# Performance work log

Hardware: AMD Instinct MI355X
Metric: run time of the kernel (lower is better)

The kernel has to match this reference:

```python
import jax, jax.numpy as jnp
import numpy as np

D_MODEL = 1024
OUTPUT_DIM = 1024
NUM_HEADS = 16
HEAD_DIM = D_MODEL // NUM_HEADS


def _xavier(key, shape):
    fan_in, fan_out = shape[1], shape[0]
    limit = float(np.sqrt(6.0 / (fan_in + fan_out)))
    return jax.random.uniform(key, shape, jnp.float32, -limit, limit)


def setup_inputs() -> dict:
    key = jax.random.key(0)
    k_h, k_q, k_k, k_o = jax.random.split(key, 4)
    H = jax.random.normal(k_h, (2, 2048, D_MODEL), dtype=jnp.float32)
    # nn.Linear weights are [out, in]; xavier_uniform on weights, default (uniform) biases left as zeros-equivalent
    Wq = _xavier(k_q, (D_MODEL, D_MODEL))
    bq = jnp.zeros((D_MODEL,), jnp.float32)
    Wk = _xavier(k_k, (D_MODEL, D_MODEL))
    bk = jnp.zeros((D_MODEL,), jnp.float32)
    Wo = _xavier(k_o, (OUTPUT_DIM, D_MODEL))
    bo = jnp.zeros((OUTPUT_DIM,), jnp.float32)
    return {"H": H, "Wq": Wq, "bq": bq, "Wk": Wk, "bk": bk, "Wo": Wo, "bo": bo}


def reference(H, Wq, bq, Wk, bk, Wo, bo):
    B, S, _ = H.shape
    Q = H @ Wq.T + bq  # [B,S,D]
    K = H @ Wk.T + bk
    # split heads -> [B,nh,S,hd]
    Qh = Q.reshape(B, S, NUM_HEADS, HEAD_DIM).transpose(0, 2, 1, 3)
    Kh = K.reshape(B, S, NUM_HEADS, HEAD_DIM).transpose(0, 2, 1, 3)
    Vh = H.reshape(B, S, NUM_HEADS, HEAD_DIM).transpose(0, 2, 1, 3)
    scale = 1.0 / jnp.sqrt(jnp.float32(HEAD_DIM))
    A = jnp.einsum('bhqd,bhkd->bhqk', Qh, Kh) * scale  # [B,nh,S,S]
    A = jax.nn.softmax(A, axis=-1)
    out = jnp.einsum('bhqk,bhkd->bhqd', A, Vh)  # [B,nh,S,hd]
    out = out.transpose(0, 2, 1, 3).reshape(B, S, D_MODEL)
    return out @ Wo.T + bo
```

## Files before the change

### kernel.cpp

```cpp
#include <hip/hip_runtime.h>
#include <stdint.h>

#define BB 2
#define SS 2048
#define DD 1024
#define NH 16
#define HD 64
#define MM 4096

typedef __bf16 bf16x8 __attribute__((ext_vector_type(8)));
typedef __bf16 bf16x4 __attribute__((ext_vector_type(4)));
typedef float  f32x4  __attribute__((ext_vector_type(4)));

__device__ __forceinline__ unsigned short f2bf(float f) {
    __bf16 h = (__bf16)f;
    return __builtin_bit_cast(unsigned short, h);
}

__device__ __forceinline__ void async_cp16(const void* g, const void* l) {
    __builtin_amdgcn_global_load_lds(
        (const __attribute__((address_space(1))) void*)(uintptr_t)g,
        (__attribute__((address_space(3))) void*)(uint32_t)(uintptr_t)l,
        16, 0, 0);
}

__device__ __forceinline__ f32x4 mfma16(bf16x8 a, bf16x8 b, f32x4 c) {
    return __builtin_amdgcn_mfma_f32_16x16x32_bf16(a, b, c, 0, 0, 0);
}

__global__ __launch_bounds__(256) void k_prep(const float* __restrict__ H,
                                              const float* __restrict__ Wq,
                                              const float* __restrict__ Wk,
                                              const float* __restrict__ Wo,
                                              unsigned short* __restrict__ Hb,
                                              unsigned short* __restrict__ Vt,
                                              unsigned short* __restrict__ Wqb,
                                              unsigned short* __restrict__ Wkb,
                                              unsigned short* __restrict__ Wob) {
    __shared__ float tile[128][68];
    const int bx = blockIdx.x;
    const int t = threadIdx.x;
    if (bx >= 512) {
        int g = bx - 512;
        const float* src; unsigned short* dst; int base;
        if (g < 512)       { src = Wq; dst = Wqb; base = g; }
        else if (g < 1024) { src = Wk; dst = Wkb; base = g - 512; }
        else               { src = Wo; dst = Wob; base = g - 1024; }
        int i = (base * 256 + t) * 8;
        float4 a = *(const float4*)(src + i);
        float4 b = *(const float4*)(src + i + 4);
        unsigned short o[8];
        o[0] = f2bf(a.x); o[1] = f2bf(a.y); o[2] = f2bf(a.z); o[3] = f2bf(a.w);
        o[4] = f2bf(b.x); o[5] = f2bf(b.y); o[6] = f2bf(b.z); o[7] = f2bf(b.w);
        *(ulonglong2*)(dst + i) = *(ulonglong2*)o;
        return;
    }
    const int sb = bx & 15, h = (bx >> 4) & 15, b = bx >> 8;
    const int col4 = t & 15;
    const int srow0 = t >> 4;
#pragma unroll
    for (int p = 0; p < 8; ++p) {
        int s = p * 16 + srow0;
        float4 v = *(const float4*)(H + (size_t)(b * SS + sb * 128 + s) * DD + h * HD + col4 * 4);
        *(float4*)&tile[s][col4 * 4] = v;
    }
    __syncthreads();
#pragma unroll
    for (int it = 0; it < 4; ++it) {
        int task = it * 256 + t;
        int s = task >> 3;
        int dg = task & 7;
        unsigned short pk[8];
#pragma unroll
        for (int j = 0; j < 8; ++j) pk[j] = f2bf(tile[s][dg * 8 + j]);
        *(ulonglong2*)(Hb + (size_t)(b * SS + sb * 128 + s) * DD + h * HD + dg * 8) = *(ulonglong2*)pk;
    }
#pragma unroll
    for (int it = 0; it < 4; ++it) {
        int task = it * 256 + t;
        int d = task >> 4;
        int sg = task & 15;
        unsigned short pk[8];
#pragma unroll
        for (int j = 0; j < 8; ++j) pk[j] = f2bf(tile[sg * 8 + j][d]);
        *(ulonglong2*)(Vt + (size_t)((b * NH + h) * HD + d) * SS + sb * 128 + sg * 8) = *(ulonglong2*)pk;
    }
}

template <int TM, bool BF16OUT>
__device__ __forceinline__ void gemm_body(const unsigned short* __restrict__ A,
                                          const unsigned short* __restrict__ Bt,
                                          const float* __restrict__ bias,
                                          void* __restrict__ Cp, float oscale) {
    constexpr int MT = TM / 32;
    constexpr int AR = (TM * 4) / 256;
    __shared__ unsigned short lsA[2][TM * 32];
    __shared__ unsigned short lsB[2][128 * 32];
    const int tid = threadIdx.x;
    const int lane = tid & 63;
    const int w = tid >> 6;
    const int wm = w & 1, wn = w >> 1;
    const int r = lane & 15, quad = lane >> 4;
    const int mBase = blockIdx.y * TM;
    const int nBase = blockIdx.x * 128;

    const unsigned short* gA[AR]; uint laOff[AR];
#pragma unroll
    for (int t = 0; t < AR; ++t) {
        int l = t * 256 + tid;
        int c = l ^ ((l >> 3) & 7);
        int row = c >> 2, kc = c & 3;
        gA[t] = A + (size_t)(mBase + row) * 1024 + kc * 8;
        laOff[t] = l * 8;
    }
    const unsigned short* gB[2]; uint lbOff[2];
#pragma unroll
    for (int t = 0; t < 2; ++t) {
        int l = t * 256 + tid;
        int c = l ^ ((l >> 3) & 7);
        int row = c >> 2, kc = c & 3;
        gB[t] = Bt + (size_t)(nBase + row) * 1024 + kc * 8;
        lbOff[t] = l * 8;
    }
    uint aOff[MT], bOff[4];
#pragma unroll
    for (int mt = 0; mt < MT; ++mt) {
        int rowA = wm * (TM / 2) + mt * 16 + r;
        int c = rowA * 4 + quad;
        aOff[mt] = (uint)((c ^ ((c >> 3) & 7)) * 8);
    }
#pragma unroll
    for (int nt = 0; nt < 4; ++nt) {
        int rowB = wn * 64 + nt * 16 + r;
        int c = rowB * 4 + quad;
        bOff[nt] = (uint)((c ^ ((c >> 3) & 7)) * 8);
    }

    f32x4 acc[MT][4];
#pragma unroll
    for (int i = 0; i < MT; ++i)
#pragma unroll
        for (int j = 0; j < 4; ++j) acc[i][j] = f32x4{0.f, 0.f, 0.f, 0.f};

    auto stage = [&](int buf) {
#pragma unroll
        for (int t = 0; t < AR; ++t) { async_cp16(gA[t], &lsA[buf][laOff[t]]); gA[t] += 32; }
#pragma unroll
        for (int t = 0; t < 2; ++t)  { async_cp16(gB[t], &lsB[buf][lbOff[t]]); gB[t] += 32; }
    };

    stage(0);
    for (int kb = 0; kb < 32; ++kb) {
        const int cur = kb & 1;
        __syncthreads();
        if (kb + 1 < 32) stage(cur ^ 1);

        bf16x8 af[MT], bf[4];
#pragma unroll
        for (int mt = 0; mt < MT; ++mt) af[mt] = *(const bf16x8*)&lsA[cur][aOff[mt]];
#pragma unroll
        for (int nt = 0; nt < 4; ++nt)  bf[nt] = *(const bf16x8*)&lsB[cur][bOff[nt]];
#pragma unroll
        for (int mt = 0; mt < MT; ++mt)
#pragma unroll
            for (int nt = 0; nt < 4; ++nt)
                acc[mt][nt] = mfma16(af[mt], bf[nt], acc[mt][nt]);
    }

    float bv[4];
#pragma unroll
    for (int nt = 0; nt < 4; ++nt) bv[nt] = bias[nBase + wn * 64 + nt * 16 + r];
#pragma unroll
    for (int mt = 0; mt < MT; ++mt)
#pragma unroll
        for (int nt = 0; nt < 4; ++nt) {
            int colg = nBase + wn * 64 + nt * 16 + r;
#pragma unroll
            for (int reg = 0; reg < 4; ++reg) {
                int rowg = mBase + wm * (TM / 2) + mt * 16 + quad * 4 + reg;
                float v = (acc[mt][nt][reg] + bv[nt]) * oscale;
                if (BF16OUT)
                    ((unsigned short*)Cp)[(size_t)rowg * 1024 + colg] = f2bf(v);
                else
                    ((float*)Cp)[(size_t)rowg * 1024 + colg] = v;
            }
        }
}

#define QSCALE 0.1803368801111137f

__global__ __launch_bounds__(256) void k_gemm_qk(const unsigned short* __restrict__ Hb,
                                                 const unsigned short* __restrict__ Wqb,
                                                 const unsigned short* __restrict__ Wkb,
                                                 const float* __restrict__ bq,
                                                 const float* __restrict__ bk,
                                                 unsigned short* __restrict__ Q,
                                                 unsigned short* __restrict__ K) {
    const unsigned short* Bt = blockIdx.z ? Wkb : Wqb;
    const float* bias = blockIdx.z ? bk : bq;
    unsigned short* C = blockIdx.z ? K : Q;
    float os = blockIdx.z ? 1.0f : QSCALE;
    gemm_body<128, true>(Hb, Bt, bias, C, os);
}

__global__ __launch_bounds__(256) void k_gemm_out(const unsigned short* __restrict__ Ctx,
                                                  const unsigned short* __restrict__ Wob,
                                                  const float* __restrict__ bo,
                                                  float* __restrict__ Out) {
    gemm_body<64, false>(Ctx, Wob, bo, Out, 1.0f);
}

__global__ __launch_bounds__(256) void k_attn(const unsigned short* __restrict__ Q,
                                              const unsigned short* __restrict__ K,
                                              const unsigned short* __restrict__ Vt,
                                              unsigned short* __restrict__ Ctx) {
    __shared__ unsigned short lsK[2][64 * 64];
    __shared__ unsigned short lsV[2][64 * 64];
    __shared__ unsigned short lsP[4 * 32 * 64];
    const int tid = threadIdx.x;
    const int lane = tid & 63;
    const int w = tid >> 6;
    const int r = lane & 15, quad = lane >> 4;
    const int qb = blockIdx.x, h = blockIdx.y, b = blockIdx.z;

    bf16x8 aq[2][2];
#pragma unroll
    for (int sub = 0; sub < 2; ++sub) {
        const int qrow = qb * 128 + w * 32 + sub * 16 + r;
        const size_t qoff = (size_t)(b * SS + qrow) * DD + h * HD;
        aq[sub][0] = *(const bf16x8*)(Q + qoff + quad * 8);
        aq[sub][1] = *(const bf16x8*)(Q + qoff + 32 + quad * 8);
    }

    f32x4 accO[2][4];
#pragma unroll
    for (int sub = 0; sub < 2; ++sub)
#pragma unroll
        for (int nt = 0; nt < 4; ++nt) accO[sub][nt] = f32x4{0.f, 0.f, 0.f, 0.f};
    float lsum[2][4] = {{0.f, 0.f, 0.f, 0.f}, {0.f, 0.f, 0.f, 0.f}};

    const unsigned short* gK[2]; const unsigned short* gV[2]; uint lO[2];
#pragma unroll
    for (int t = 0; t < 2; ++t) {
        int l = t * 256 + tid;
        int c = l ^ ((l >> 3) & 7);
        int row = c >> 3, kc = c & 7;
        int srow = 4 * (row & 15) + (row >> 4);
        gK[t] = K + (size_t)(b * SS + srow) * DD + h * HD + kc * 8;
        gV[t] = Vt + (size_t)((b * NH + h) * HD + row) * SS + kc * 8;
        lO[t] = l * 8;
    }
    uint off[2][4];
#pragma unroll
    for (int t = 0; t < 2; ++t)
#pragma unroll
        for (int nt = 0; nt < 4; ++nt) {
            int rowX = nt * 16 + r;
            int c = rowX * 8 + t * 4 + quad;
            off[t][nt] = (uint)((c ^ ((c >> 3) & 7)) * 8);
        }
    uint pw[4], pr[2];
#pragma unroll
    for (int reg = 0; reg < 4; ++reg) {
        int prow = quad * 4 + reg;
        pw[reg] = (uint)(prow * 64 + ((r >> 1) ^ (prow & 7)) * 8 + (r & 1) * 4);
    }
#pragma unroll
    for (int t = 0; t < 2; ++t)
        pr[t] = (uint)(r * 64 + ((4 * t + quad) ^ (r & 7)) * 8);
    unsigned short* Pw = lsP + w * 2048;

    auto stage = [&](int buf) {
#pragma unroll
        for (int t = 0; t < 2; ++t) {
            async_cp16(gK[t], &lsK[buf][lO[t]]); gK[t] += 64 * DD;
            async_cp16(gV[t], &lsV[buf][lO[t]]); gV[t] += 64;
        }
    };

    stage(0);
    for (int kt = 0; kt < 32; ++kt) {
        const int cur = kt & 1;
        __syncthreads();
        if (kt + 1 < 32) stage(cur ^ 1);

        f32x4 s[2][4];
#pragma unroll
        for (int sub = 0; sub < 2; ++sub)
#pragma unroll
            for (int nt = 0; nt < 4; ++nt) s[sub][nt] = f32x4{0.f, 0.f, 0.f, 0.f};
#pragma unroll
        for (int t = 0; t < 2; ++t)
#pragma unroll
            for (int nt = 0; nt < 4; ++nt) {
                bf16x8 bk = *(const bf16x8*)&lsK[cur][off[t][nt]];
                s[0][nt] = mfma16(aq[0][t], bk, s[0][nt]);
                s[1][nt] = mfma16(aq[1][t], bk, s[1][nt]);
            }

#pragma unroll
        for (int sub = 0; sub < 2; ++sub)
#pragma unroll
            for (int reg = 0; reg < 4; ++reg) {
                float p0 = __builtin_amdgcn_exp2f(s[sub][0][reg]);
                float p1 = __builtin_amdgcn_exp2f(s[sub][1][reg]);
                float p2 = __builtin_amdgcn_exp2f(s[sub][2][reg]);
                float p3 = __builtin_amdgcn_exp2f(s[sub][3][reg]);
                lsum[sub][reg] += (p0 + p1) + (p2 + p3);
                bf16x4 pk = {(__bf16)p0, (__bf16)p1, (__bf16)p2, (__bf16)p3};
                *(bf16x4*)&Pw[sub * 1024 + pw[reg]] = pk;
            }

#pragma unroll
        for (int t = 0; t < 2; ++t) {
            bf16x8 ap0 = *(const bf16x8*)&Pw[pr[t]];
            bf16x8 ap1 = *(const bf16x8*)&Pw[1024 + pr[t]];
#pragma unroll
            for (int nt = 0; nt < 4; ++nt) {
                bf16x8 bv = *(const bf16x8*)&lsV[cur][off[t][nt]];
                accO[0][nt] = mfma16(ap0, bv, accO[0][nt]);
                accO[1][nt] = mfma16(ap1, bv, accO[1][nt]);
            }
        }
    }

#pragma unroll
    for (int sub = 0; sub < 2; ++sub) {
        float linv[4];
#pragma unroll
        for (int reg = 0; reg < 4; ++reg) {
            float l = lsum[sub][reg];
            l += __shfl_xor(l, 1);
            l += __shfl_xor(l, 2);
            l += __shfl_xor(l, 4);
            l += __shfl_xor(l, 8);
            linv[reg] = 1.0f / l;
        }
#pragma unroll
        for (int nt = 0; nt < 4; ++nt) {
            int d = nt * 16 + r;
#pragma unroll
            for (int reg = 0; reg < 4; ++reg) {
                int qr = qb * 128 + w * 32 + sub * 16 + quad * 4 + reg;
                Ctx[(size_t)(b * SS + qr) * DD + h * HD + d] = f2bf(accO[sub][nt][reg] * linv[reg]);
            }
        }
    }
}

extern "C" void kernel_launch(void* const* d_in, const int* in_sizes, int n_in,
                              void* d_out, int out_size, void* d_ws, size_t ws_size,
                              hipStream_t stream) {
    (void)in_sizes; (void)n_in; (void)out_size; (void)ws_size;
    const float* H  = (const float*)d_in[0];
    const float* Wq = (const float*)d_in[1];
    const float* bq = (const float*)d_in[2];
    const float* Wk = (const float*)d_in[3];
    const float* bk = (const float*)d_in[4];
    const float* Wo = (const float*)d_in[5];
    const float* bo = (const float*)d_in[6];
    float* Out = (float*)d_out;

    char* ws = (char*)d_ws;
    unsigned short* Hb  = (unsigned short*)(ws);
    unsigned short* Qb  = (unsigned short*)(ws + 8388608);
    unsigned short* Kb  = (unsigned short*)(ws + 16777216);
    unsigned short* Ctx = (unsigned short*)(ws + 25165824);
    unsigned short* Vt  = (unsigned short*)(ws + 33554432);
    unsigned short* Wqb = (unsigned short*)(ws + 41943040);
    unsigned short* Wkb = (unsigned short*)(ws + 44040192);
    unsigned short* Wob = (unsigned short*)(ws + 46137344);

    k_prep<<<dim3(2048), dim3(256), 0, stream>>>(H, Wq, Wk, Wo, Hb, Vt, Wqb, Wkb, Wob);
    k_gemm_qk<<<dim3(8, 32, 2), dim3(256), 0, stream>>>(Hb, Wqb, Wkb, bq, bk, Qb, Kb);
    k_attn<<<dim3(16, NH, BB), dim3(256), 0, stream>>>(Qb, Kb, Vt, Ctx);
    k_gemm_out<<<dim3(8, 64, 1), dim3(256), 0, stream>>>(Ctx, Wob, bo, Out);
}
```

Before: 181.3 us.

## Double GEMM K-tile to 64 and load attention K/V directly to registers

The GEMM body now stages 64-wide K slices instead of 32, halving the number of barrier-separated iterations and doubling the MFMA work per sync. The attention kernel drops the shared-memory staging of K and V and has each wave load its K and V fragments straight from global memory into registers, prefetching the next K tile. This removes the per-tile __syncthreads and LDS traffic. In exchange, each of the four waves fetches the same K/V data separately, so global/L2 traffic rises, and both register pressure and GEMM LDS usage grow.

```diff
diff --git a/kernel.cpp b/kernel.cpp
--- a/kernel.cpp
+++ b/kernel.cpp
@@ -93,9 +93,9 @@
                                           const float* __restrict__ bias,
                                           void* __restrict__ Cp, float oscale) {
     constexpr int MT = TM / 32;
-    constexpr int AR = (TM * 4) / 256;
-    __shared__ unsigned short lsA[2][TM * 32];
-    __shared__ unsigned short lsB[2][128 * 32];
+    constexpr int AR = TM / 32;
+    __shared__ unsigned short lsA[2][TM * 64];
+    __shared__ unsigned short lsB[2][128 * 64];
     const int tid = threadIdx.x;
     const int lane = tid & 63;
     const int w = tid >> 6;
@@ -109,31 +109,34 @@
     for (int t = 0; t < AR; ++t) {
         int l = t * 256 + tid;
         int c = l ^ ((l >> 3) & 7);
-        int row = c >> 2, kc = c & 3;
+        int row = c >> 3, kc = c & 7;
         gA[t] = A + (size_t)(mBase + row) * 1024 + kc * 8;
         laOff[t] = l * 8;
     }
-    const unsigned short* gB[2]; uint lbOff[2];
-#pragma unroll
-    for (int t = 0; t < 2; ++t) {
+    const unsigned short* gB[4]; uint lbOff[4];
+#pragma unroll
+    for (int t = 0; t < 4; ++t) {
         int l = t * 256 + tid;
         int c = l ^ ((l >> 3) & 7);
-        int row = c >> 2, kc = c & 3;
+        int row = c >> 3, kc = c & 7;
         gB[t] = Bt + (size_t)(nBase + row) * 1024 + kc * 8;
         lbOff[t] = l * 8;
     }
-    uint aOff[MT], bOff[4];
-#pragma unroll
-    for (int mt = 0; mt < MT; ++mt) {
-        int rowA = wm * (TM / 2) + mt * 16 + r;
-        int c = rowA * 4 + quad;
-        aOff[mt] = (uint)((c ^ ((c >> 3) & 7)) * 8);
-    }
-#pragma unroll
-    for (int nt = 0; nt < 4; ++nt) {
-        int rowB = wn * 64 + nt * 16 + r;
-        int c = rowB * 4 + quad;
-        bOff[nt] = (uint)((c ^ ((c >> 3) & 7)) * 8);
+    uint aOff[2][MT], bOff[2][4];
+#pragma unroll
+    for (int hh = 0; hh < 2; ++hh) {
+#pragma unroll
+        for (int mt = 0; mt < MT; ++mt) {
+            int rowA = wm * (TM / 2) + mt * 16 + r;
+            int c = rowA * 8 + hh * 4 + quad;
+            aOff[hh][mt] = (uint)((c ^ ((c >> 3) & 7)) * 8);
+        }
+#pragma unroll
+        for (int nt = 0; nt < 4; ++nt) {
+            int rowB = wn * 64 + nt * 16 + r;
+            int c = rowB * 8 + hh * 4 + quad;
+            bOff[hh][nt] = (uint)((c ^ ((c >> 3) & 7)) * 8);
+        }
     }
 
     f32x4 acc[MT][4];
@@ -144,27 +147,30 @@
 
     auto stage = [&](int buf) {
 #pragma unroll
-        for (int t = 0; t < AR; ++t) { async_cp16(gA[t], &lsA[buf][laOff[t]]); gA[t] += 32; }
-#pragma unroll
-        for (int t = 0; t < 2; ++t)  { async_cp16(gB[t], &lsB[buf][lbOff[t]]); gB[t] += 32; }
+        for (int t = 0; t < AR; ++t) { async_cp16(gA[t], &lsA[buf][laOff[t]]); gA[t] += 64; }
+#pragma unroll
+        for (int t = 0; t < 4; ++t)  { async_cp16(gB[t], &lsB[buf][lbOff[t]]); gB[t] += 64; }
     };
 
     stage(0);
-    for (int kb = 0; kb < 32; ++kb) {
+    for (int kb = 0; kb < 16; ++kb) {
         const int cur = kb & 1;
         __syncthreads();
-        if (kb + 1 < 32) stage(cur ^ 1);
-
-        bf16x8 af[MT], bf[4];
-#pragma unroll
-        for (int mt = 0; mt < MT; ++mt) af[mt] = *(const bf16x8*)&lsA[cur][aOff[mt]];
-#pragma unroll
-        for (int nt = 0; nt < 4; ++nt)  bf[nt] = *(const bf16x8*)&lsB[cur][bOff[nt]];
-#pragma unroll
-        for (int mt = 0; mt < MT; ++mt)
-#pragma unroll
-            for (int nt = 0; nt < 4; ++nt)
-                acc[mt][nt] = mfma16(af[mt], bf[nt], acc[mt][nt]);
+        if (kb + 1 < 16) stage(cur ^ 1);
+
+#pragma unroll
+        for (int hh = 0; hh < 2; ++hh) {
+            bf16x8 af[MT], bf[4];
+#pragma unroll
+            for (int mt = 0; mt < MT; ++mt) af[mt] = *(const bf16x8*)&lsA[cur][aOff[hh][mt]];
+#pragma unroll
+            for (int nt = 0; nt < 4; ++nt)  bf[nt] = *(const bf16x8*)&lsB[cur][bOff[hh][nt]];
+#pragma unroll
+            for (int mt = 0; mt < MT; ++mt)
+#pragma unroll
+                for (int nt = 0; nt < 4; ++nt)
+                    acc[mt][nt] = mfma16(af[mt], bf[nt], acc[mt][nt]);
+        }
     }
 
     float bv[4];
@@ -214,9 +220,7 @@
                                               const unsigned short* __restrict__ K,
                                               const unsigned short* __restrict__ Vt,
                                               unsigned short* __restrict__ Ctx) {
-    __shared__ unsigned short lsK[2][64 * 64];
-    __shared__ unsigned short lsV[2][64 * 64];
-    __shared__ unsigned short lsP[4 * 32 * 64];
+    __shared__ unsigned short lsP[4 * 2048];
     const int tid = threadIdx.x;
     const int lane = tid & 63;
     const int w = tid >> 6;
@@ -239,25 +243,15 @@
         for (int nt = 0; nt < 4; ++nt) accO[sub][nt] = f32x4{0.f, 0.f, 0.f, 0.f};
     float lsum[2][4] = {{0.f, 0.f, 0.f, 0.f}, {0.f, 0.f, 0.f, 0.f}};
 
-    const unsigned short* gK[2]; const unsigned short* gV[2]; uint lO[2];
-#pragma unroll
-    for (int t = 0; t < 2; ++t) {
-        int l = t * 256 + tid;
-        int c = l ^ ((l >> 3) & 7);
-        int row = c >> 3, kc = c & 7;
-        int srow = 4 * (row & 15) + (row >> 4);
-        gK[t] = K + (size_t)(b * SS + srow) * DD + h * HD + kc * 8;
-        gV[t] = Vt + (size_t)((b * NH + h) * HD + row) * SS + kc * 8;
-        lO[t] = l * 8;
-    }
-    uint off[2][4];
+    const unsigned short* Kb_ = K + (size_t)b * SS * DD + h * HD;
+    const unsigned short* Vb_ = Vt + (size_t)(b * NH + h) * HD * SS;
+    uint kOff[2][4], vOff[2][4];
 #pragma unroll
     for (int t = 0; t < 2; ++t)
 #pragma unroll
         for (int nt = 0; nt < 4; ++nt) {
-            int rowX = nt * 16 + r;
-            int c = rowX * 8 + t * 4 + quad;
-            off[t][nt] = (uint)((c ^ ((c >> 3) & 7)) * 8);
+            kOff[t][nt] = (uint)((4 * r + nt) * DD + t * 32 + quad * 8);
+            vOff[t][nt] = (uint)((nt * 16 + r) * SS + t * 32 + quad * 8);
         }
     uint pw[4], pr[2];
 #pragma unroll
@@ -270,19 +264,30 @@
         pr[t] = (uint)(r * 64 + ((4 * t + quad) ^ (r & 7)) * 8);
     unsigned short* Pw = lsP + w * 2048;
 
-    auto stage = [&](int buf) {
-#pragma unroll
-        for (int t = 0; t < 2; ++t) {
-            async_cp16(gK[t], &lsK[buf][lO[t]]); gK[t] += 64 * DD;
-            async_cp16(gV[t], &lsV[buf][lO[t]]); gV[t] += 64;
-        }
-    };
-
-    stage(0);
+    bf16x8 kf[2][2][4];
+#pragma unroll
+    for (int t = 0; t < 2; ++t)
+#pragma unroll
+        for (int nt = 0; nt < 4; ++nt)
+            kf[0][t][nt] = *(const bf16x8*)(Kb_ + kOff[t][nt]);
+
+#pragma unroll 2
     for (int kt = 0; kt < 32; ++kt) {
         const int cur = kt & 1;
-        __syncthreads();
-        if (kt + 1 < 32) stage(cur ^ 1);
+        const uint kbase_n = (uint)(((kt + 1) & 31) * 64) * DD;
+        const uint vbase   = (uint)(kt * 64);
+
+        bf16x8 vf[2][4];
+#pragma unroll
+        for (int t = 0; t < 2; ++t)
+#pragma unroll
+            for (int nt = 0; nt < 4; ++nt)
+                vf[t][nt] = *(const bf16x8*)(Vb_ + vbase + vOff[t][nt]);
+#pragma unroll
+        for (int t = 0; t < 2; ++t)
+#pragma unroll
+            for (int nt = 0; nt < 4; ++nt)
+                kf[cur ^ 1][t][nt] = *(const bf16x8*)(Kb_ + kbase_n + kOff[t][nt]);
 
         f32x4 s[2][4];
 #pragma unroll
@@ -293,7 +298,7 @@
         for (int t = 0; t < 2; ++t)
 #pragma unroll
             for (int nt = 0; nt < 4; ++nt) {
-                bf16x8 bk = *(const bf16x8*)&lsK[cur][off[t][nt]];
+                bf16x8 bk = kf[cur][t][nt];
                 s[0][nt] = mfma16(aq[0][t], bk, s[0][nt]);
                 s[1][nt] = mfma16(aq[1][t], bk, s[1][nt]);
             }
@@ -317,7 +322,7 @@
             bf16x8 ap1 = *(const bf16x8*)&Pw[1024 + pr[t]];
 #pragma unroll
             for (int nt = 0; nt < 4; ++nt) {
-                bf16x8 bv = *(const bf16x8*)&lsV[cur][off[t][nt]];
+                bf16x8 bv = vf[t][nt];
                 accO[0][nt] = mfma16(ap0, bv, accO[0][nt]);
                 accO[1][nt] = mfma16(ap1, bv, accO[1][nt]);
             }
```

Measured after the change: 245.1 us. +35.2%, slower.
